# Kernel optimization log

Hardware: AMD Instinct MI355X
Metric: run time of the kernel (lower is better)

Reference implementation:

```python
import jax, jax.numpy as jnp
import numpy as np

N = 20000
E = 320000
D_IN = 256
D = 128
H = 4
L = 2
NUM_CLASSES = 7
LN_EPS = 1e-5


def setup_inputs() -> dict:
    key = jax.random.key(0)
    ks = jax.random.split(key, 12)
    inp = {}
    inp["x"] = jax.random.normal(ks[0], (N, D_IN), dtype=jnp.float32)
    inp["edge_index"] = jax.random.randint(ks[1], (2, E), 0, N, dtype=jnp.int32)
    inp["W_in"] = jax.random.normal(ks[2], (D_IN, D), dtype=jnp.float32) / np.sqrt(D_IN)
    inp["b_in"] = jnp.zeros((D,), jnp.float32)
    inp["Wq"] = jax.random.normal(ks[3], (L, D, H * D), dtype=jnp.float32) / np.sqrt(D)
    inp["bq"] = jnp.zeros((L, H * D), jnp.float32)
    inp["Wk"] = jax.random.normal(ks[4], (L, D, H * D), dtype=jnp.float32) / np.sqrt(D)
    inp["bk"] = jnp.zeros((L, H * D), jnp.float32)
    inp["Wv"] = jax.random.normal(ks[5], (L, D, H * D), dtype=jnp.float32) / np.sqrt(D)
    inp["bv"] = jnp.zeros((L, H * D), jnp.float32)
    inp["Wskip"] = jax.random.normal(ks[6], (L, D, D), dtype=jnp.float32) / np.sqrt(D)
    inp["bskip"] = jnp.zeros((L, D), jnp.float32)
    inp["ln_g"] = jnp.ones((L, D), jnp.float32)
    inp["ln_b"] = jnp.zeros((L, D), jnp.float32)
    inp["Wc"] = jax.random.normal(ks[7], (D, NUM_CLASSES), dtype=jnp.float32) / np.sqrt(D)
    inp["bc"] = jnp.zeros((NUM_CLASSES,), jnp.float32)
    return inp


def degree_pe(edge_index):
    # degree of source nodes (edge_index[0]), then sinusoidal encoding of the degree
    deg = jax.ops.segment_sum(jnp.ones((E,), jnp.float32), edge_index[0], num_segments=N)
    i = jnp.arange(D, dtype=jnp.float32)
    freq = deg[:, None] / jnp.power(10000.0, i / D)[None, :]  # [N, D]
    return jnp.where((jnp.arange(D) % 2 == 0)[None, :], jnp.sin(freq), jnp.cos(freq))


def transformer_conv(xf, edge_index, Wq, bq, Wk, bk, Wv, bv, Wskip, bskip):
    # PyG TransformerConv: heads=H, concat=False (mean over heads), root_weight=True
    src, dst = edge_index[0], edge_index[1]
    q = (xf @ Wq + bq).reshape(N, H, D)
    k = (xf @ Wk + bk).reshape(N, H, D)
    v = (xf @ Wv + bv).reshape(N, H, D)
    qe = q[dst]                        # [E, H, D]
    ke = k[src]
    ve = v[src]
    scores = jnp.sum(qe * ke, axis=-1) / np.sqrt(D)  # [E, H]
    m = jax.ops.segment_max(scores, dst, num_segments=N)        # [N, H]
    p = jnp.exp(scores - m[dst])
    s = jax.ops.segment_sum(p, dst, num_segments=N)              # [N, H]
    alpha = p / (s[dst] + 1e-16)
    agg = jax.ops.segment_sum(alpha[:, :, None] * ve, dst, num_segments=N)  # [N, H, D]
    out = jnp.mean(agg, axis=1)       # concat=False -> average heads
    return out + xf @ Wskip + bskip   # root skip connection


def layer_norm(x, g, b):
    mu = jnp.mean(x, axis=-1, keepdims=True)
    var = jnp.mean(jnp.square(x - mu), axis=-1, keepdims=True)
    return (x - mu) * jax.lax.rsqrt(var + LN_EPS) * g + b


def reference(x, edge_index, W_in, b_in, Wq, bq, Wk, bk, Wv, bv, Wskip, bskip, ln_g, ln_b, Wc, bc):
    h = x @ W_in + b_in
    h = h + degree_pe(edge_index)
    for l in range(L):
        h_new = transformer_conv(h, edge_index, Wq[l], bq[l], Wk[l], bk[l], Wv[l], bv[l], Wskip[l], bskip[l])
        h = layer_norm(h + h_new, ln_g[l], ln_b[l])
        if l < L - 1:
            h = jax.nn.relu(h)
    return h @ Wc + bc  # [N, num_classes]
```

## Files before the change

### kernel.cpp

```cpp
#include <hip/hip_runtime.h>
#include <math.h>

#define NN 20000
#define EE 320000
#define DIN 256
#define DD 128
#define HHEADS 4
#define NCLS 7

typedef __attribute__((ext_vector_type(8))) __bf16 bf16x8;
typedef __attribute__((ext_vector_type(4))) float f32x4;
typedef __attribute__((ext_vector_type(2))) float f32x2;

__device__ __forceinline__ unsigned short f2bf(float f) {
  union { float f; unsigned int u; } c; c.f = f;
  unsigned int r = c.u + 0x7fffu + ((c.u >> 16) & 1u);
  return (unsigned short)(r >> 16);
}
__device__ __forceinline__ __bf16 f2bf16(float f) {
  union { unsigned short u; __bf16 b; } cv; cv.u = f2bf(f); return cv.b;
}
__device__ __forceinline__ unsigned char fp8enc(float v) {
  return (unsigned char)(__builtin_amdgcn_cvt_pk_fp8_f32(v, 0.f, 0, false) & 0xff);
}
__device__ __forceinline__ void fp8x4_dec(unsigned int w, float* o) {
  f32x2 lo = __builtin_amdgcn_cvt_pk_f32_fp8((int)w, false);
  f32x2 hi = __builtin_amdgcn_cvt_pk_f32_fp8((int)w, true);
  o[0] = lo[0]; o[1] = lo[1]; o[2] = hi[0]; o[3] = hi[1];
}

__global__ void zero_ints(int* __restrict__ p, int n) {
  int i = blockIdx.x * blockDim.x + threadIdx.x;
  if (i < n) p[i] = 0;
}

__global__ void count_kernel(const int* __restrict__ ei, int* __restrict__ deg_src,
                             int* __restrict__ cnt_dst) {
  int e = blockIdx.x * blockDim.x + threadIdx.x;
  if (e >= EE) return;
  atomicAdd(&deg_src[ei[e]], 1);
  atomicAdd(&cnt_dst[ei[EE + e]], 1);
}

__global__ __launch_bounds__(1024) void scan_kernel(const int* __restrict__ cnt,
                                                    int* __restrict__ row_ptr,
                                                    int* __restrict__ fillp) {
  __shared__ int wsum[16];
  __shared__ int carry_s;
  const int tid = threadIdx.x;
  const int wid = tid >> 6, lane = tid & 63;
  if (tid == 0) carry_s = 0;
  __syncthreads();
  for (int base = 0; base < NN; base += 1024) {
    int i = base + tid;
    int x = (i < NN) ? cnt[i] : 0;
    int v = x;
#pragma unroll
    for (int off = 1; off < 64; off <<= 1) {
      int t = __shfl_up(v, off);
      if (lane >= off) v += t;
    }
    if (lane == 63) wsum[wid] = v;
    __syncthreads();
    int woff = 0;
    for (int w = 0; w < wid; ++w) woff += wsum[w];
    int excl = carry_s + woff + v - x;
    if (i < NN) { row_ptr[i] = excl; fillp[i] = excl; }
    __syncthreads();
    if (tid == 1023) carry_s += woff + v;
    __syncthreads();
  }
  if (tid == 0) row_ptr[NN] = EE;
}

__global__ void scatter_kernel(const int* __restrict__ ei, int* __restrict__ fillp,
                               int* __restrict__ ssrc) {
  int e = blockIdx.x * blockDim.x + threadIdx.x;
  if (e >= EE) return;
  int s = ei[e], d = ei[EE + e];
  int pos = atomicAdd(&fillp[d], 1);
  ssrc[pos] = s;
}

__global__ void pack_weights(const float* __restrict__ W_in, const float* __restrict__ Wq,
                             const float* __restrict__ Wk, const float* __restrict__ Wv,
                             const float* __restrict__ Wsk, const float* __restrict__ Wc,
                             __bf16* __restrict__ WT) {
  int idx = blockIdx.x * blockDim.x + threadIdx.x;
  if (idx >= 475136) return;
  float val;
  if (idx < 32768) {
    int m = idx >> 8, k = idx & 255;
    val = W_in[k * 128 + m];
  } else if (idx < 458752) {
    int t = idx - 32768;
    int l = t / 212992; int t2 = t - l * 212992;
    int r = t2 >> 7, kk = t2 & 127;
    if (r < 512)       val = Wq[l * 65536 + kk * 512 + r];
    else if (r < 1024) val = Wk[l * 65536 + kk * 512 + (r - 512)];
    else if (r < 1536) val = Wv[l * 65536 + kk * 512 + (r - 1024)];
    else               val = Wsk[l * 16384 + kk * 128 + (r - 1536)];
  } else {
    int t = idx - 458752;
    int r = t >> 7, kk = t & 127;
    val = (r < NCLS) ? Wc[kk * NCLS + r] : 0.f;
  }
  WT[idx] = f2bf16(val);
}

__global__ void pack_bias(const float* __restrict__ bq, const float* __restrict__ bk,
                          const float* __restrict__ bv, const float* __restrict__ bsk,
                          const float* __restrict__ bc, float* __restrict__ bcomb,
                          float* __restrict__ bcpad) {
  int idx = blockIdx.x * blockDim.x + threadIdx.x;
  if (idx < 3328) {
    int l = idx / 1664, r = idx % 1664;
    float v;
    if (r < 512)       v = bq[l * 512 + r];
    else if (r < 1024) v = bk[l * 512 + (r - 512)];
    else if (r < 1536) v = bv[l * 512 + (r - 1024)];
    else               v = bsk[l * 128 + (r - 1536)];
    bcomb[idx] = v;
  } else if (idx < 3456) {
    int r = idx - 3328;
    bcpad[r] = (r < NCLS) ? bc[r] : 0.f;
  }
}

__global__ __launch_bounds__(256) void mfma_gemm_in(
    const float* __restrict__ A, const __bf16* __restrict__ BT,
    const float* __restrict__ bias, float* __restrict__ o_f32,
    __bf16* __restrict__ o_bf0, const int* __restrict__ deg) {
  constexpr int K = 256;
  __shared__ __attribute__((aligned(16))) __bf16 As[64][136];
  __shared__ __attribute__((aligned(16))) __bf16 Bs[128][136];
  const int tid = threadIdx.x;
  const int brow = blockIdx.x * 64;
  const int bcol = 0;
  const int wave = tid >> 6, lane = tid & 63;
  const int wm = wave & 1, wn = wave >> 1;
  const int lm = lane & 15, lk = (lane >> 4) * 8;
  const int srow16 = tid >> 4;
  const int sc8 = (tid & 15) * 8;
  f32x4 acc[2][4] = {};
  for (int k0 = 0; k0 < K; k0 += 128) {
    if (k0) __syncthreads();
#pragma unroll
    for (int t = 0; t < 4; ++t) {
      int row = t * 16 + srow16;
      int arow = brow + row;
      arow = (arow < NN) ? arow : (NN - 1);
      const float* ap = A + (size_t)arow * K + k0 + sc8;
      float4 a0 = *(const float4*)ap, a1 = *(const float4*)(ap + 4);
      uint4 w;
      w.x = (unsigned)f2bf(a0.x) | ((unsigned)f2bf(a0.y) << 16);
      w.y = (unsigned)f2bf(a0.z) | ((unsigned)f2bf(a0.w) << 16);
      w.z = (unsigned)f2bf(a1.x) | ((unsigned)f2bf(a1.y) << 16);
      w.w = (unsigned)f2bf(a1.z) | ((unsigned)f2bf(a1.w) << 16);
      *reinterpret_cast<uint4*>(&As[row][sc8]) = w;
    }
#pragma unroll
    for (int t = 0; t < 8; ++t) {
      int row = t * 16 + srow16;
      *reinterpret_cast<uint4*>(&Bs[row][sc8]) =
          *reinterpret_cast<const uint4*>(BT + (size_t)(bcol + row) * K + k0 + sc8);
    }
    __syncthreads();
#pragma unroll
    for (int ks = 0; ks < 4; ++ks) {
      bf16x8 af[2], bfr[4];
#pragma unroll
      for (int i = 0; i < 2; ++i)
        af[i] = *reinterpret_cast<const bf16x8*>(&As[wm * 32 + i * 16 + lm][ks * 32 + lk]);
#pragma unroll
      for (int j = 0; j < 4; ++j)
        bfr[j] = *reinterpret_cast<const bf16x8*>(&Bs[wn * 64 + j * 16 + lm][ks * 32 + lk]);
#pragma unroll
      for (int i = 0; i < 2; ++i)
#pragma unroll
        for (int j = 0; j < 4; ++j)
          acc[i][j] = __builtin_amdgcn_mfma_f32_16x16x32_bf16(af[i], bfr[j], acc[i][j], 0, 0, 0);
    }
  }
#pragma unroll
  for (int i = 0; i < 2; ++i) {
#pragma unroll
    for (int j = 0; j < 4; ++j) {
      const int col = bcol + wn * 64 + j * 16 + lm;
      const float bb = bias[col];
#pragma unroll
      for (int r = 0; r < 4; ++r) {
        const int row = brow + wm * 32 + i * 16 + (lane >> 4) * 4 + r;
        if (row >= NN) continue;
        float val = acc[i][j][r] + bb;
        float dg = (float)deg[row];
        float freq = dg * __expf(-0.07195578415606394f * (float)col);
        val += (col & 1) ? __cosf(freq) : __sinf(freq);
        o_f32[(size_t)row * DD + col] = val;
        o_bf0[(size_t)row * DD + col] = f2bf16(val);
      }
    }
  }
}

template <int MODE>
__global__ __launch_bounds__(256) void mfma_gemm_nk(
    const __bf16* __restrict__ A, const __bf16* __restrict__ BT,
    const float* __restrict__ bias, const float* __restrict__ resid,
    float* __restrict__ o_f32, __bf16* __restrict__ o_bf0,
    unsigned char* __restrict__ o_fp8, float* __restrict__ o_hs) {
  __shared__ __attribute__((aligned(16))) __bf16 Bs[128][136];
  const int tid = threadIdx.x;
  const int brow = blockIdx.x * 64;
  const int bcol = blockIdx.y * 128;
  const int wave = tid >> 6, lane = tid & 63;
  const int wm = wave & 1, wn = wave >> 1;
  const int lm = lane & 15, lk = (lane >> 4) * 8;
  const int srow16 = tid >> 4;
  const int sc8 = (tid & 15) * 8;

  uint4 breg[8];
#pragma unroll
  for (int t = 0; t < 8; ++t)
    breg[t] = *reinterpret_cast<const uint4*>(BT + (size_t)(bcol + t * 16 + srow16) * 128 + sc8);

  bf16x8 af[2][4];
#pragma unroll
  for (int i = 0; i < 2; ++i) {
    int row = brow + wm * 32 + i * 16 + lm;
    row = (row < NN) ? row : (NN - 1);
    const __bf16* ap = A + (size_t)row * 128 + lk;
#pragma unroll
    for (int ks = 0; ks < 4; ++ks)
      af[i][ks] = *reinterpret_cast<const bf16x8*>(ap + ks * 32);
  }

#pragma unroll
  for (int t = 0; t < 8; ++t)
    *reinterpret_cast<uint4*>(&Bs[t * 16 + srow16][sc8]) = breg[t];
  __syncthreads();

  f32x4 acc[2][4] = {};
#pragma unroll
  for (int ks = 0; ks < 4; ++ks) {
    bf16x8 bfr[4];
#pragma unroll
    for (int j = 0; j < 4; ++j)
      bfr[j] = *reinterpret_cast<const bf16x8*>(&Bs[wn * 64 + j * 16 + lm][ks * 32 + lk]);
#pragma unroll
    for (int i = 0; i < 2; ++i)
#pragma unroll
      for (int j = 0; j < 4; ++j)
        acc[i][j] = __builtin_amdgcn_mfma_f32_16x16x32_bf16(af[i][ks], bfr[j], acc[i][j], 0, 0, 0);
  }

#pragma unroll
  for (int i = 0; i < 2; ++i) {
#pragma unroll
    for (int j = 0; j < 4; ++j) {
      const int col = bcol + wn * 64 + j * 16 + lm;
      const float bb = bias[col];
#pragma unroll
      for (int r = 0; r < 4; ++r) {
        const int row = brow + wm * 32 + i * 16 + (lane >> 4) * 4 + r;
        if (row >= NN) continue;
        float val = acc[i][j][r] + bb;
        if constexpr (MODE == 1) {
          if (col < 512) {
            o_bf0[(size_t)row * 512 + col] = f2bf16(val);
          } else if (col < 1024) {
            int dim = col - 512;
            o_fp8[(size_t)row * 1024 + (dim >> 3) * 16 + (dim & 7)] = fp8enc(val);
          } else if (col < 1536) {
            int dim = col - 1024;
            o_fp8[(size_t)row * 1024 + (dim >> 3) * 16 + 8 + (dim & 7)] = fp8enc(val);
          } else {
            o_hs[(size_t)row * DD + (col - 1536)] =
                val + resid[(size_t)row * DD + (col - 1536)];
          }
        } else {
          if (col < NCLS) o_f32[(size_t)row * NCLS + col] = val;
        }
      }
    }
  }
}

__device__ __forceinline__ uint4 loadkv(const unsigned char* __restrict__ kv,
                                        const int* __restrict__ ssrc, int ee, int lane) {
  return *reinterpret_cast<const uint4*>(kv + (size_t)ssrc[ee] * 1024 + lane * 16);
}
__device__ __forceinline__ float qdot8(const float (&qv)[8], unsigned kx, unsigned ky) {
  float kd[8];
  fp8x4_dec(kx, kd);
  fp8x4_dec(ky, kd + 4);
  float d = qv[0] * kd[0];
  d = fmaf(qv[1], kd[1], d);
  d = fmaf(qv[2], kd[2], d);
  d = fmaf(qv[3], kd[3], d);
  d = fmaf(qv[4], kd[4], d);
  d = fmaf(qv[5], kd[5], d);
  d = fmaf(qv[6], kd[6], d);
  d = fmaf(qv[7], kd[7], d);
  d += __shfl_xor(d, 1);
  d += __shfl_xor(d, 2);
  d += __shfl_xor(d, 4);
  d += __shfl_xor(d, 8);
  return d;
}
__device__ __forceinline__ void accum8(float (&a)[8], float& m, float& s, float sc,
                                       unsigned vz, unsigned vw) {
  if (sc > m) {
    float c = __expf(m - sc);
    s *= c;
#pragma unroll
    for (int d = 0; d < 8; ++d) a[d] *= c;
    m = sc;
  }
  float w = __expf(sc - m);
  s += w;
  float vd[8];
  fp8x4_dec(vz, vd);
  fp8x4_dec(vw, vd + 4);
#pragma unroll
  for (int d = 0; d < 8; ++d) a[d] = fmaf(w, vd[d], a[d]);
}

__global__ __launch_bounds__(256) void attn_fused(
    const __bf16* __restrict__ qb, const unsigned char* __restrict__ kv,
    const float* __restrict__ hs,
    const int* __restrict__ row_ptr, const int* __restrict__ ssrc,
    const float* __restrict__ ln_g, const float* __restrict__ ln_b,
    float* __restrict__ h_out, __bf16* __restrict__ hb_out, int relu_flag) {
  const int node = blockIdx.x * 4 + (threadIdx.x >> 6);
  const int lane = threadIdx.x & 63;
  const int grp = lane >> 4, l16 = lane & 15;
  const int e0 = row_ptr[node], e1 = row_ptr[node + 1];
  const float scale = 0.088388347648318447f;

  float qv[8];
  {
    uint4 qw = *reinterpret_cast<const uint4*>(qb + (size_t)node * 512 + lane * 8);
    union { unsigned u; float f; } c;
    c.u = qw.x << 16; qv[0] = c.f; c.u = qw.x & 0xffff0000u; qv[1] = c.f;
    c.u = qw.y << 16; qv[2] = c.f; c.u = qw.y & 0xffff0000u; qv[3] = c.f;
    c.u = qw.z << 16; qv[4] = c.f; c.u = qw.z & 0xffff0000u; qv[5] = c.f;
    c.u = qw.w << 16; qv[6] = c.f; c.u = qw.w & 0xffff0000u; qv[7] = c.f;
  }
  float m = -INFINITY, s = 0.f;
  float a[8] = {0.f, 0.f, 0.f, 0.f, 0.f, 0.f, 0.f, 0.f};

  uint4 w0, w1, w2, w3;
  if (e0 + 0 < e1) w0 = loadkv(kv, ssrc, e0 + 0, lane);
  if (e0 + 1 < e1) w1 = loadkv(kv, ssrc, e0 + 1, lane);
  if (e0 + 2 < e1) w2 = loadkv(kv, ssrc, e0 + 2, lane);
  if (e0 + 3 < e1) w3 = loadkv(kv, ssrc, e0 + 3, lane);
  int e = e0;
  while (e < e1) {
    {
      float sc = qdot8(qv, w0.x, w0.y) * scale;
      unsigned vz = w0.z, vw = w0.w;
      if (e + 4 < e1) w0 = loadkv(kv, ssrc, e + 4, lane);
      accum8(a, m, s, sc, vz, vw);
    }
    if (e + 1 < e1) {
      float sc = qdot8(qv, w1.x, w1.y) * scale;
      unsigned vz = w1.z, vw = w1.w;
      if (e + 5 < e1) w1 = loadkv(kv, ssrc, e + 5, lane);
      accum8(a, m, s, sc, vz, vw);
    }
    if (e + 2 < e1) {
      float sc = qdot8(qv, w2.x, w2.y) * scale;
      unsigned vz = w2.z, vw = w2.w;
      if (e + 6 < e1) w2 = loadkv(kv, ssrc, e + 6, lane);
      accum8(a, m, s, sc, vz, vw);
    }
    if (e + 3 < e1) {
      float sc = qdot8(qv, w3.x, w3.y) * scale;
      unsigned vz = w3.z, vw = w3.w;
      if (e + 7 < e1) w3 = loadkv(kv, ssrc, e + 7, lane);
      accum8(a, m, s, sc, vz, vw);
    }
    e += 4;
  }

  float inv = 0.25f / (s + 1e-16f);
#pragma unroll
  for (int d = 0; d < 8; ++d) {
    float ad = a[d] * inv;
    ad += __shfl_xor(ad, 16);
    ad += __shfl_xor(ad, 32);
    a[d] = ad;
  }

  const float4* hp = reinterpret_cast<const float4*>(hs + (size_t)node * DD + l16 * 8);
  float4 h0 = hp[0], h1 = hp[1];
  float val[8];
  val[0] = a[0] + h0.x; val[1] = a[1] + h0.y; val[2] = a[2] + h0.z; val[3] = a[3] + h0.w;
  val[4] = a[4] + h1.x; val[5] = a[5] + h1.y; val[6] = a[6] + h1.z; val[7] = a[7] + h1.w;
  float sum = 0.f, sq = 0.f;
#pragma unroll
  for (int d = 0; d < 8; ++d) { sum += val[d]; sq += val[d] * val[d]; }
  sum += __shfl_xor(sum, 1); sq += __shfl_xor(sq, 1);
  sum += __shfl_xor(sum, 2); sq += __shfl_xor(sq, 2);
  sum += __shfl_xor(sum, 4); sq += __shfl_xor(sq, 4);
  sum += __shfl_xor(sum, 8); sq += __shfl_xor(sq, 8);
  float mu = sum * (1.f / 128.f);
  float var = sq * (1.f / 128.f) - mu * mu;
  float rstd = rsqrtf(var + 1e-5f);

  const float4* gp = reinterpret_cast<const float4*>(ln_g + l16 * 8);
  const float4* bp = reinterpret_cast<const float4*>(ln_b + l16 * 8);
  float4 g0 = gp[0], g1 = gp[1];
  float4 b0 = bp[0], b1 = bp[1];
  float y[8];
  y[0] = (val[0] - mu) * rstd * g0.x + b0.x;
  y[1] = (val[1] - mu) * rstd * g0.y + b0.y;
  y[2] = (val[2] - mu) * rstd * g0.z + b0.z;
  y[3] = (val[3] - mu) * rstd * g0.w + b0.w;
  y[4] = (val[4] - mu) * rstd * g1.x + b1.x;
  y[5] = (val[5] - mu) * rstd * g1.y + b1.y;
  y[6] = (val[6] - mu) * rstd * g1.z + b1.z;
  y[7] = (val[7] - mu) * rstd * g1.w + b1.w;
  if (relu_flag) {
#pragma unroll
    for (int d = 0; d < 8; ++d) y[d] = fmaxf(y[d], 0.f);
  }
  if (grp == 0) {
    float4* op = reinterpret_cast<float4*>(h_out + (size_t)node * DD + l16 * 8);
    op[0] = make_float4(y[0], y[1], y[2], y[3]);
    op[1] = make_float4(y[4], y[5], y[6], y[7]);
  } else if (grp == 1) {
    uint4 w;
    w.x = (unsigned)f2bf(y[0]) | ((unsigned)f2bf(y[1]) << 16);
    w.y = (unsigned)f2bf(y[2]) | ((unsigned)f2bf(y[3]) << 16);
    w.z = (unsigned)f2bf(y[4]) | ((unsigned)f2bf(y[5]) << 16);
    w.w = (unsigned)f2bf(y[6]) | ((unsigned)f2bf(y[7]) << 16);
    *reinterpret_cast<uint4*>(hb_out + (size_t)node * DD + l16 * 8) = w;
  }
}

extern "C" void kernel_launch(void* const* d_in, const int* in_sizes, int n_in,
                              void* d_out, int out_size, void* d_ws, size_t ws_size,
                              hipStream_t stream) {
  const float* x    = (const float*)d_in[0];
  const int*   ei   = (const int*)d_in[1];
  const float* W_in = (const float*)d_in[2];
  const float* b_in = (const float*)d_in[3];
  const float* Wq   = (const float*)d_in[4];
  const float* bq   = (const float*)d_in[5];
  const float* Wk   = (const float*)d_in[6];
  const float* bk   = (const float*)d_in[7];
  const float* Wv   = (const float*)d_in[8];
  const float* bv   = (const float*)d_in[9];
  const float* Wsk  = (const float*)d_in[10];
  const float* bsk  = (const float*)d_in[11];
  const float* ln_g = (const float*)d_in[12];
  const float* ln_b = (const float*)d_in[13];
  const float* Wc   = (const float*)d_in[14];
  const float* bc   = (const float*)d_in[15];
  float* out = (float*)d_out;

  char* ws = (char*)d_ws;
  size_t off = 0;
  float*  hA    = (float*)(ws + off);  off += (size_t)NN * DD * 4;
  float*  hB    = (float*)(ws + off);  off += (size_t)NN * DD * 4;
  __bf16* qb    = (__bf16*)(ws + off); off += (size_t)NN * 512 * 2;
  unsigned char* kvb = (unsigned char*)(ws + off); off += (size_t)NN * 1024;
  float*  hsb   = (float*)(ws + off);  off += (size_t)NN * DD * 4;
  __bf16* hb0   = (__bf16*)(ws + off); off += (size_t)NN * DD * 2;
  __bf16* hb1   = (__bf16*)(ws + off); off += (size_t)NN * DD * 2;
  __bf16* WT    = (__bf16*)(ws + off); off += (size_t)475136 * 2;
  float*  bcomb = (float*)(ws + off);  off += (size_t)3328 * 4;
  float*  bcpad = (float*)(ws + off);  off += (size_t)128 * 4;
  int* deg      = (int*)(ws + off);    off += (size_t)NN * 4;
  int* cnt      = (int*)(ws + off);    off += (size_t)NN * 4;
  int* fillp    = (int*)(ws + off);    off += (size_t)NN * 4;
  int* row_ptr  = (int*)(ws + off);    off += (size_t)(NN + 1) * 4;
  int* ssrc     = (int*)(ws + off);    off += (size_t)EE * 4;

  __bf16* W_inT = WT;
  __bf16* W2T   = WT + 32768;
  __bf16* WcT   = WT + 458752;

  zero_ints<<<(2 * NN + 255) / 256, 256, 0, stream>>>(deg, 2 * NN);
  count_kernel<<<(EE + 255) / 256, 256, 0, stream>>>(ei, deg, cnt);
  scan_kernel<<<1, 1024, 0, stream>>>(cnt, row_ptr, fillp);
  scatter_kernel<<<(EE + 255) / 256, 256, 0, stream>>>(ei, fillp, ssrc);

  pack_weights<<<(475136 + 255) / 256, 256, 0, stream>>>(W_in, Wq, Wk, Wv, Wsk, Wc, WT);
  pack_bias<<<(3456 + 255) / 256, 256, 0, stream>>>(bq, bk, bv, bsk, bc, bcomb, bcpad);

  mfma_gemm_in<<<dim3((NN + 63) / 64, 1), 256, 0, stream>>>(x, W_inT, b_in, hA, hb0, deg);

  const float*  h_in_l[2]   = {hA, hB};
  float*        h_out_l[2]  = {hB, hA};
  const __bf16* hb_in_l[2]  = {hb0, hb1};
  __bf16*       hb_out_l[2] = {hb1, hb0};

  for (int l = 0; l < 2; ++l) {
    dim3 gqkv((NN + 63) / 64, 13);
    mfma_gemm_nk<1><<<gqkv, 256, 0, stream>>>(hb_in_l[l], W2T + (size_t)l * 212992,
                                              bcomb + (size_t)l * 1664, h_in_l[l],
                                              nullptr, qb, kvb, hsb);
    attn_fused<<<NN / 4, 256, 0, stream>>>(qb, kvb, hsb, row_ptr, ssrc,
                                           ln_g + (size_t)l * DD, ln_b + (size_t)l * DD,
                                           h_out_l[l], hb_out_l[l], (l == 0) ? 1 : 0);
  }

  mfma_gemm_nk<2><<<dim3((NN + 63) / 64, 1), 256, 0, stream>>>(
      hb0, WcT, bcpad, nullptr, out, nullptr, nullptr, nullptr);
}
```

Before: 320.5 us.

## Retile QKV GEMM over 256 rows, shrink classifier GEMM, pack attention math

The QKV projection GEMM now has each block loop over four 64-row tiles while reusing one shared-memory weight tile, and it prefetches the next A fragments into a register double buffer. The classifier GEMM becomes a dedicated kernel with a 16-column padded weight instead of 128 columns, which cuts wasted MFMA work and weight packing. The attention inner loops switch to packed float2 arithmetic with direct packed FP8 conversion. The trade-off is fewer QKV blocks (lower occupancy and parallelism) and more register pressure from the double-buffered fragments.

```diff
diff --git a/kernel.cpp b/kernel.cpp
--- a/kernel.cpp
+++ b/kernel.cpp
@@ -22,11 +22,6 @@
 }
 __device__ __forceinline__ unsigned char fp8enc(float v) {
   return (unsigned char)(__builtin_amdgcn_cvt_pk_fp8_f32(v, 0.f, 0, false) & 0xff);
-}
-__device__ __forceinline__ void fp8x4_dec(unsigned int w, float* o) {
-  f32x2 lo = __builtin_amdgcn_cvt_pk_f32_fp8((int)w, false);
-  f32x2 hi = __builtin_amdgcn_cvt_pk_f32_fp8((int)w, true);
-  o[0] = lo[0]; o[1] = lo[1]; o[2] = hi[0]; o[3] = hi[1];
 }
 
 __global__ void zero_ints(int* __restrict__ p, int n) {
@@ -87,7 +82,7 @@
                              const float* __restrict__ Wsk, const float* __restrict__ Wc,
                              __bf16* __restrict__ WT) {
   int idx = blockIdx.x * blockDim.x + threadIdx.x;
-  if (idx >= 475136) return;
+  if (idx >= 460800) return;
   float val;
   if (idx < 32768) {
     int m = idx >> 8, k = idx & 255;
@@ -121,7 +116,7 @@
     else if (r < 1536) v = bv[l * 512 + (r - 1024)];
     else               v = bsk[l * 128 + (r - 1536)];
     bcomb[idx] = v;
-  } else if (idx < 3456) {
+  } else if (idx < 3344) {
     int r = idx - 3328;
     bcpad[r] = (r < NCLS) ? bc[r] : 0.f;
   }
@@ -136,7 +131,6 @@
   __shared__ __attribute__((aligned(16))) __bf16 Bs[128][136];
   const int tid = threadIdx.x;
   const int brow = blockIdx.x * 64;
-  const int bcol = 0;
   const int wave = tid >> 6, lane = tid & 63;
   const int wm = wave & 1, wn = wave >> 1;
   const int lm = lane & 15, lk = (lane >> 4) * 8;
@@ -163,7 +157,7 @@
     for (int t = 0; t < 8; ++t) {
       int row = t * 16 + srow16;
       *reinterpret_cast<uint4*>(&Bs[row][sc8]) =
-          *reinterpret_cast<const uint4*>(BT + (size_t)(bcol + row) * K + k0 + sc8);
+          *reinterpret_cast<const uint4*>(BT + (size_t)row * K + k0 + sc8);
     }
     __syncthreads();
 #pragma unroll
@@ -186,7 +180,7 @@
   for (int i = 0; i < 2; ++i) {
 #pragma unroll
     for (int j = 0; j < 4; ++j) {
-      const int col = bcol + wn * 64 + j * 16 + lm;
+      const int col = wn * 64 + j * 16 + lm;
       const float bb = bias[col];
 #pragma unroll
       for (int r = 0; r < 4; ++r) {
@@ -203,71 +197,74 @@
   }
 }
 
-template <int MODE>
-__global__ __launch_bounds__(256) void mfma_gemm_nk(
+__global__ __launch_bounds__(256) void mfma_gemm_qkv(
     const __bf16* __restrict__ A, const __bf16* __restrict__ BT,
     const float* __restrict__ bias, const float* __restrict__ resid,
-    float* __restrict__ o_f32, __bf16* __restrict__ o_bf0,
-    unsigned char* __restrict__ o_fp8, float* __restrict__ o_hs) {
+    __bf16* __restrict__ o_q, unsigned char* __restrict__ o_fp8,
+    float* __restrict__ o_hs) {
   __shared__ __attribute__((aligned(16))) __bf16 Bs[128][136];
   const int tid = threadIdx.x;
-  const int brow = blockIdx.x * 64;
+  const int row0 = blockIdx.x * 256;
   const int bcol = blockIdx.y * 128;
   const int wave = tid >> 6, lane = tid & 63;
   const int wm = wave & 1, wn = wave >> 1;
-  const int lm = lane & 15, lk = (lane >> 4) * 8;
+  const int lm = lane & 15, lk = (lane >> 4) * 8, l4 = (lane >> 4) * 4;
   const int srow16 = tid >> 4;
   const int sc8 = (tid & 15) * 8;
 
-  uint4 breg[8];
 #pragma unroll
   for (int t = 0; t < 8; ++t)
-    breg[t] = *reinterpret_cast<const uint4*>(BT + (size_t)(bcol + t * 16 + srow16) * 128 + sc8);
-
-  bf16x8 af[2][4];
-#pragma unroll
-  for (int i = 0; i < 2; ++i) {
-    int row = brow + wm * 32 + i * 16 + lm;
-    row = (row < NN) ? row : (NN - 1);
-    const __bf16* ap = A + (size_t)row * 128 + lk;
-#pragma unroll
-    for (int ks = 0; ks < 4; ++ks)
-      af[i][ks] = *reinterpret_cast<const bf16x8*>(ap + ks * 32);
-  }
-
-#pragma unroll
-  for (int t = 0; t < 8; ++t)
-    *reinterpret_cast<uint4*>(&Bs[t * 16 + srow16][sc8]) = breg[t];
+    *reinterpret_cast<uint4*>(&Bs[t * 16 + srow16][sc8]) =
+        *reinterpret_cast<const uint4*>(BT + (size_t)(bcol + t * 16 + srow16) * 128 + sc8);
   __syncthreads();
 
-  f32x4 acc[2][4] = {};
-#pragma unroll
-  for (int ks = 0; ks < 4; ++ks) {
-    bf16x8 bfr[4];
-#pragma unroll
-    for (int j = 0; j < 4; ++j)
-      bfr[j] = *reinterpret_cast<const bf16x8*>(&Bs[wn * 64 + j * 16 + lm][ks * 32 + lk]);
-#pragma unroll
-    for (int i = 0; i < 2; ++i)
+  auto loadA = [&](bf16x8 (&dst)[2][4], int base) {
+#pragma unroll
+    for (int i = 0; i < 2; ++i) {
+      int row = base + wm * 32 + i * 16 + lm;
+      row = (row < NN) ? row : (NN - 1);
+      const __bf16* ap = A + (size_t)row * 128 + lk;
+#pragma unroll
+      for (int ks = 0; ks < 4; ++ks) dst[i][ks] = *reinterpret_cast<const bf16x8*>(ap + ks * 32);
+    }
+  };
+
+  bf16x8 afA[2][4], afB[2][4];
+  loadA(afA, row0);
+#pragma unroll
+  for (int t = 0; t < 4; ++t) {
+    bf16x8(&af)[2][4] = (t & 1) ? afB : afA;
+    bf16x8(&nxt)[2][4] = (t & 1) ? afA : afB;
+    if (t < 3) loadA(nxt, row0 + (t + 1) * 64);
+    const int trow = row0 + t * 64;
+
+    f32x4 acc[2][4] = {};
+#pragma unroll
+    for (int ks = 0; ks < 4; ++ks) {
+      bf16x8 bfr[4];
 #pragma unroll
       for (int j = 0; j < 4; ++j)
-        acc[i][j] = __builtin_amdgcn_mfma_f32_16x16x32_bf16(af[i][ks], bfr[j], acc[i][j], 0, 0, 0);
-  }
-
-#pragma unroll
-  for (int i = 0; i < 2; ++i) {
-#pragma unroll
-    for (int j = 0; j < 4; ++j) {
-      const int col = bcol + wn * 64 + j * 16 + lm;
-      const float bb = bias[col];
-#pragma unroll
-      for (int r = 0; r < 4; ++r) {
-        const int row = brow + wm * 32 + i * 16 + (lane >> 4) * 4 + r;
-        if (row >= NN) continue;
-        float val = acc[i][j][r] + bb;
-        if constexpr (MODE == 1) {
+        bfr[j] = *reinterpret_cast<const bf16x8*>(&Bs[wn * 64 + j * 16 + lm][ks * 32 + lk]);
+#pragma unroll
+      for (int i = 0; i < 2; ++i)
+#pragma unroll
+        for (int j = 0; j < 4; ++j)
+          acc[i][j] = __builtin_amdgcn_mfma_f32_16x16x32_bf16(af[i][ks], bfr[j], acc[i][j], 0, 0, 0);
+    }
+
+#pragma unroll
+    for (int i = 0; i < 2; ++i) {
+#pragma unroll
+      for (int j = 0; j < 4; ++j) {
+        const int col = bcol + wn * 64 + j * 16 + lm;
+        const float bb = bias[col];
+#pragma unroll
+        for (int r = 0; r < 4; ++r) {
+          const int row = trow + wm * 32 + i * 16 + l4 + r;
+          if (row >= NN) continue;
+          float val = acc[i][j][r] + bb;
           if (col < 512) {
-            o_bf0[(size_t)row * 512 + col] = f2bf16(val);
+            o_q[(size_t)row * 512 + col] = f2bf16(val);
           } else if (col < 1024) {
             int dim = col - 512;
             o_fp8[(size_t)row * 1024 + (dim >> 3) * 16 + (dim & 7)] = fp8enc(val);
@@ -278,9 +275,51 @@
             o_hs[(size_t)row * DD + (col - 1536)] =
                 val + resid[(size_t)row * DD + (col - 1536)];
           }
-        } else {
-          if (col < NCLS) o_f32[(size_t)row * NCLS + col] = val;
         }
+      }
+    }
+  }
+}
+
+__global__ __launch_bounds__(256) void mfma_gemm_cls(
+    const __bf16* __restrict__ A, const __bf16* __restrict__ BT,
+    const float* __restrict__ bias, float* __restrict__ out) {
+  __shared__ __attribute__((aligned(16))) __bf16 Bs[16][136];
+  const int tid = threadIdx.x;
+  const int wave = tid >> 6, lane = tid & 63;
+  const int lm = lane & 15, lk = (lane >> 4) * 8, l4 = (lane >> 4) * 4;
+  const int brow = blockIdx.x * 128 + wave * 32;
+  if (tid < 256) {
+    int srow = tid >> 4, sc8 = (tid & 15) * 8;
+    *reinterpret_cast<uint4*>(&Bs[srow][sc8]) =
+        *reinterpret_cast<const uint4*>(BT + (size_t)srow * 128 + sc8);
+  }
+  __syncthreads();
+  bf16x8 af[2][4];
+#pragma unroll
+  for (int i = 0; i < 2; ++i) {
+    int row = brow + i * 16 + lm;
+    row = (row < NN) ? row : (NN - 1);
+    const __bf16* ap = A + (size_t)row * 128 + lk;
+#pragma unroll
+    for (int ks = 0; ks < 4; ++ks) af[i][ks] = *reinterpret_cast<const bf16x8*>(ap + ks * 32);
+  }
+  f32x4 acc[2] = {};
+#pragma unroll
+  for (int ks = 0; ks < 4; ++ks) {
+    bf16x8 bfr = *reinterpret_cast<const bf16x8*>(&Bs[lm][ks * 32 + lk]);
+#pragma unroll
+    for (int i = 0; i < 2; ++i)
+      acc[i] = __builtin_amdgcn_mfma_f32_16x16x32_bf16(af[i][ks], bfr, acc[i], 0, 0, 0);
+  }
+  if (lm < NCLS) {
+    const float bb = bias[lm];
+#pragma unroll
+    for (int i = 0; i < 2; ++i) {
+#pragma unroll
+      for (int r = 0; r < 4; ++r) {
+        int row = brow + i * 16 + l4 + r;
+        if (row < NN) out[(size_t)row * NCLS + lm] = acc[i][r] + bb;
       }
     }
   }
@@ -290,40 +329,43 @@
                                         const int* __restrict__ ssrc, int ee, int lane) {
   return *reinterpret_cast<const uint4*>(kv + (size_t)ssrc[ee] * 1024 + lane * 16);
 }
-__device__ __forceinline__ float qdot8(const float (&qv)[8], unsigned kx, unsigned ky) {
-  float kd[8];
-  fp8x4_dec(kx, kd);
-  fp8x4_dec(ky, kd + 4);
-  float d = qv[0] * kd[0];
-  d = fmaf(qv[1], kd[1], d);
-  d = fmaf(qv[2], kd[2], d);
-  d = fmaf(qv[3], kd[3], d);
-  d = fmaf(qv[4], kd[4], d);
-  d = fmaf(qv[5], kd[5], d);
-  d = fmaf(qv[6], kd[6], d);
-  d = fmaf(qv[7], kd[7], d);
+__device__ __forceinline__ float qdot8(const f32x2 (&qv)[4], unsigned kx, unsigned ky) {
+  f32x2 kd0 = __builtin_amdgcn_cvt_pk_f32_fp8((int)kx, false);
+  f32x2 kd1 = __builtin_amdgcn_cvt_pk_f32_fp8((int)kx, true);
+  f32x2 kd2 = __builtin_amdgcn_cvt_pk_f32_fp8((int)ky, false);
+  f32x2 kd3 = __builtin_amdgcn_cvt_pk_f32_fp8((int)ky, true);
+  f32x2 d2 = qv[0] * kd0;
+  d2 = qv[1] * kd1 + d2;
+  d2 = qv[2] * kd2 + d2;
+  d2 = qv[3] * kd3 + d2;
+  float d = d2[0] + d2[1];
   d += __shfl_xor(d, 1);
   d += __shfl_xor(d, 2);
   d += __shfl_xor(d, 4);
   d += __shfl_xor(d, 8);
   return d;
 }
-__device__ __forceinline__ void accum8(float (&a)[8], float& m, float& s, float sc,
+__device__ __forceinline__ void accum8(f32x2 (&a)[4], float& m, float& s, float sc,
                                        unsigned vz, unsigned vw) {
   if (sc > m) {
     float c = __expf(m - sc);
+    f32x2 c2 = {c, c};
     s *= c;
 #pragma unroll
-    for (int d = 0; d < 8; ++d) a[d] *= c;
+    for (int d = 0; d < 4; ++d) a[d] *= c2;
     m = sc;
   }
   float w = __expf(sc - m);
   s += w;
-  float vd[8];
-  fp8x4_dec(vz, vd);
-  fp8x4_dec(vw, vd + 4);
-#pragma unroll
-  for (int d = 0; d < 8; ++d) a[d] = fmaf(w, vd[d], a[d]);
+  f32x2 w2 = {w, w};
+  f32x2 vd0 = __builtin_amdgcn_cvt_pk_f32_fp8((int)vz, false);
+  f32x2 vd1 = __builtin_amdgcn_cvt_pk_f32_fp8((int)vz, true);
+  f32x2 vd2 = __builtin_amdgcn_cvt_pk_f32_fp8((int)vw, false);
+  f32x2 vd3 = __builtin_amdgcn_cvt_pk_f32_fp8((int)vw, true);
+  a[0] = w2 * vd0 + a[0];
+  a[1] = w2 * vd1 + a[1];
+  a[2] = w2 * vd2 + a[2];
+  a[3] = w2 * vd3 + a[3];
 }
 
 __global__ __launch_bounds__(256) void attn_fused(
@@ -338,17 +380,17 @@
   const int e0 = row_ptr[node], e1 = row_ptr[node + 1];
   const float scale = 0.088388347648318447f;
 
-  float qv[8];
+  f32x2 qv[4];
   {
     uint4 qw = *reinterpret_cast<const uint4*>(qb + (size_t)node * 512 + lane * 8);
     union { unsigned u; float f; } c;
-    c.u = qw.x << 16; qv[0] = c.f; c.u = qw.x & 0xffff0000u; qv[1] = c.f;
-    c.u = qw.y << 16; qv[2] = c.f; c.u = qw.y & 0xffff0000u; qv[3] = c.f;
-    c.u = qw.z << 16; qv[4] = c.f; c.u = qw.z & 0xffff0000u; qv[5] = c.f;
-    c.u = qw.w << 16; qv[6] = c.f; c.u = qw.w & 0xffff0000u; qv[7] = c.f;
+    c.u = qw.x << 16; qv[0][0] = c.f; c.u = qw.x & 0xffff0000u; qv[0][1] = c.f;
+    c.u = qw.y << 16; qv[1][0] = c.f; c.u = qw.y & 0xffff0000u; qv[1][1] = c.f;
+    c.u = qw.z << 16; qv[2][0] = c.f; c.u = qw.z & 0xffff0000u; qv[2][1] = c.f;
+    c.u = qw.w << 16; qv[3][0] = c.f; c.u = qw.w & 0xffff0000u; qv[3][1] = c.f;
   }
   float m = -INFINITY, s = 0.f;
-  float a[8] = {0.f, 0.f, 0.f, 0.f, 0.f, 0.f, 0.f, 0.f};
+  f32x2 a[4] = {};
 
   uint4 w0, w1, w2, w3;
   if (e0 + 0 < e1) w0 = loadkv(kv, ssrc, e0 + 0, lane);
@@ -385,19 +427,20 @@
   }
 
   float inv = 0.25f / (s + 1e-16f);
+  float am[8];
 #pragma unroll
   for (int d = 0; d < 8; ++d) {
-    float ad = a[d] * inv;
+    float ad = a[d >> 1][d & 1] * inv;
     ad += __shfl_xor(ad, 16);
     ad += __shfl_xor(ad, 32);
-    a[d] = ad;
+    am[d] = ad;
   }
 
   const float4* hp = reinterpret_cast<const float4*>(hs + (size_t)node * DD + l16 * 8);
   float4 h0 = hp[0], h1 = hp[1];
   float val[8];
-  val[0] = a[0] + h0.x; val[1] = a[1] + h0.y; val[2] = a[2] + h0.z; val[3] = a[3] + h0.w;
-  val[4] = a[4] + h1.x; val[5] = a[5] + h1.y; val[6] = a[6] + h1.z; val[7] = a[7] + h1.w;
+  val[0] = am[0] + h0.x; val[1] = am[1] + h0.y; val[2] = am[2] + h0.z; val[3] = am[3] + h0.w;
+  val[4] = am[4] + h1.x; val[5] = am[5] + h1.y; val[6] = am[6] + h1.z; val[7] = am[7] + h1.w;
   float sum = 0.f, sq = 0.f;
 #pragma unroll
   for (int d = 0; d < 8; ++d) { sum += val[d]; sq += val[d] * val[d]; }
@@ -470,9 +513,9 @@
   float*  hsb   = (float*)(ws + off);  off += (size_t)NN * DD * 4;
   __bf16* hb0   = (__bf16*)(ws + off); off += (size_t)NN * DD * 2;
   __bf16* hb1   = (__bf16*)(ws + off); off += (size_t)NN * DD * 2;
-  __bf16* WT    = (__bf16*)(ws + off); off += (size_t)475136 * 2;
+  __bf16* WT    = (__bf16*)(ws + off); off += (size_t)460800 * 2;
   float*  bcomb = (float*)(ws + off);  off += (size_t)3328 * 4;
-  float*  bcpad = (float*)(ws + off);  off += (size_t)128 * 4;
+  float*  bcpad = (float*)(ws + off);  off += (size_t)16 * 4;
   int* deg      = (int*)(ws + off);    off += (size_t)NN * 4;
   int* cnt      = (int*)(ws + off);    off += (size_t)NN * 4;
   int* fillp    = (int*)(ws + off);    off += (size_t)NN * 4;
@@ -488,8 +531,8 @@
   scan_kernel<<<1, 1024, 0, stream>>>(cnt, row_ptr, fillp);
   scatter_kernel<<<(EE + 255) / 256, 256, 0, stream>>>(ei, fillp, ssrc);
 
-  pack_weights<<<(475136 + 255) / 256, 256, 0, stream>>>(W_in, Wq, Wk, Wv, Wsk, Wc, WT);
-  pack_bias<<<(3456 + 255) / 256, 256, 0, stream>>>(bq, bk, bv, bsk, bc, bcomb, bcpad);
+  pack_weights<<<(460800 + 255) / 256, 256, 0, stream>>>(W_in, Wq, Wk, Wv, Wsk, Wc, WT);
+  pack_bias<<<(3344 + 255) / 256, 256, 0, stream>>>(bq, bk, bv, bsk, bc, bcomb, bcpad);
 
   mfma_gemm_in<<<dim3((NN + 63) / 64, 1), 256, 0, stream>>>(x, W_inT, b_in, hA, hb0, deg);
 
@@ -499,15 +542,14 @@
   __bf16*       hb_out_l[2] = {hb1, hb0};
 
   for (int l = 0; l < 2; ++l) {
-    dim3 gqkv((NN + 63) / 64, 13);
-    mfma_gemm_nk<1><<<gqkv, 256, 0, stream>>>(hb_in_l[l], W2T + (size_t)l * 212992,
-                                              bcomb + (size_t)l * 1664, h_in_l[l],
-                                              nullptr, qb, kvb, hsb);
+    dim3 gqkv((NN + 255) / 256, 13);
+    mfma_gemm_qkv<<<gqkv, 256, 0, stream>>>(hb_in_l[l], W2T + (size_t)l * 212992,
+                                            bcomb + (size_t)l * 1664, h_in_l[l],
+                                            qb, kvb, hsb);
     attn_fused<<<NN / 4, 256, 0, stream>>>(qb, kvb, hsb, row_ptr, ssrc,
                                            ln_g + (size_t)l * DD, ln_b + (size_t)l * DD,
                                            h_out_l[l], hb_out_l[l], (l == 0) ? 1 : 0);
   }
 
-  mfma_gemm_nk<2><<<dim3((NN + 63) / 64, 1), 256, 0, stream>>>(
-      hb0, WcT, bcpad, nullptr, out, nullptr, nullptr, nullptr);
-}
+  mfma_gemm_cls<<<dim3((NN + 127) / 128, 1), 256, 0, stream>>>(hb0, WcT, bcpad, out);
+}
```

New measurement: 387.0 us. 20.7% more time.
